# Kernel tuning notes

Hardware: AMD Instinct MI355X
Metric: run time of the kernel (lower is better)

The kernel has to match this reference:

```python
import jax, jax.numpy as jnp
import numpy as np
from jax import lax

EPS = 1e-5

def quantize_ternary(w):
    # scale = mean(|w|).clamp_min(1e-5) computed on detached weight
    scale = jnp.maximum(jnp.mean(jnp.abs(lax.stop_gradient(w))), EPS)
    ws = w / scale
    # STE: forward uses round+clamp, backward is identity in ws
    wq = lax.stop_gradient(jnp.clip(jnp.round(ws), -1.0, 1.0) - ws) + ws
    return wq * scale

def conv2d(x, w, b):
    # x: [N,C,H,W], w: [O,I,kh,kw], stride 1, pad 1 -> same spatial size
    out = lax.conv_general_dilated(
        x, w, window_strides=(1, 1), padding=[(1, 1), (1, 1)],
        dimension_numbers=("NCHW", "OIHW", "NCHW"))
    return out + b[None, :, None, None]

def setup_inputs() -> dict:
    key = jax.random.key(0)
    k1, k2, k3, k4, k5 = jax.random.split(key, 5)
    N, C_in, C_out, H, W, K = 16, 64, 64, 128, 128, 3
    fan_in = C_in * K * K
    bound = 1.0 / np.sqrt(fan_in)
    x = jax.random.normal(k1, (N, C_in, H, W), dtype=jnp.float32)
    w = jax.random.uniform(k2, (C_out, C_in, K, K), minval=-bound, maxval=bound, dtype=jnp.float32)
    b = jax.random.uniform(k3, (C_out,), minval=-bound, maxval=bound, dtype=jnp.float32)
    # growth child: kaiming-uniform-like init scaled by 0.01, zero bias
    w_child = jax.random.uniform(k4, (C_out, C_in, K, K), minval=-bound, maxval=bound, dtype=jnp.float32) * 0.01
    b_child = jnp.zeros((C_out,), dtype=jnp.float32)
    gate = jnp.zeros((1,), dtype=jnp.float32)  # growth_gate buffer
    return {"x": x, "w": w, "b": b, "w_child": w_child, "b_child": b_child, "gate": gate}

def reference(x, w, b, w_child, b_child, gate):
    out = conv2d(x, quantize_ternary(w), b)
    child_out = conv2d(x, quantize_ternary(w_child), b_child)
    g = jax.nn.sigmoid(gate)  # shape [1], broadcasts
    return out + g * child_out
```

## Files before the change

### kernel.cpp

```cpp
#include <hip/hip_runtime.h>
#include <math.h>


typedef __attribute__((ext_vector_type(8))) short short8;
typedef __attribute__((ext_vector_type(4))) float float4v;

__device__ inline unsigned short f2bf(float f) {
  union { float f; unsigned u; } v; v.f = f;
  unsigned u = v.u;
  return (unsigned short)((u + 0x7FFFu + ((u >> 16) & 1u)) >> 16);
}

__global__ __launch_bounds__(1024) void reduce_abs_part(const float* __restrict__ w,
                                                        const float* __restrict__ wc,
                                                        double* __restrict__ part) {
  const int base = blockIdx.x * 4096 + threadIdx.x;
  double a = 0.0, c = 0.0;
#pragma unroll
  for (int i = 0; i < 4; ++i) {
    a += (double)fabsf(w[base + i * 1024]);
    c += (double)fabsf(wc[base + i * 1024]);
  }
#pragma unroll
  for (int off = 32; off > 0; off >>= 1) {
    a += __shfl_down(a, off);
    c += __shfl_down(c, off);
  }
  __shared__ double sa[16], sc[16];
  int wv = threadIdx.x >> 6;
  if ((threadIdx.x & 63) == 0) { sa[wv] = a; sc[wv] = c; }
  __syncthreads();
  if (threadIdx.x == 0) {
    double ta = 0.0, tc = 0.0;
#pragma unroll
    for (int i = 0; i < 16; ++i) { ta += sa[i]; tc += sc[i]; }
    part[blockIdx.x] = ta;
    part[9 + blockIdx.x] = tc;
  }
}

__global__ void quant_combine(const float* __restrict__ w, const float* __restrict__ wc,
                              const float* __restrict__ b, const float* __restrict__ bc,
                              const float* __restrict__ gate, const double* __restrict__ part,
                              unsigned short* __restrict__ wq, float* __restrict__ beff) {
  double s0 = 0.0, s1 = 0.0;
#pragma unroll
  for (int i = 0; i < 9; ++i) { s0 += part[i]; s1 += part[9 + i]; }
  const float sw = fmaxf((float)(s0 * (1.0 / 36864.0)), 1e-5f);
  const float sc = fmaxf((float)(s1 * (1.0 / 36864.0)), 1e-5f);
  const float g = 1.0f / (1.0f + expf(-gate[0]));
  int idx = blockIdx.x * 256 + threadIdx.x;
  int tap = idx >> 12;
  int oc = (idx >> 6) & 63;
  int ci = idx & 63;
  int src = oc * 576 + ci * 9 + tap;
  float q1 = fminf(1.f, fmaxf(-1.f, rintf(w[src] / sw))) * sw;
  float q2 = fminf(1.f, fmaxf(-1.f, rintf(wc[src] / sc))) * sc;
  wq[idx] = f2bf(q1 + g * q2);
  if (idx < 64) beff[idx] = b[idx] + g * bc[idx];
}

__global__ __launch_bounds__(256, 2) void conv_fused(
    const float* __restrict__ x, const unsigned short* __restrict__ wq,
    const float* __restrict__ beff, float* __restrict__ out) {
  extern __shared__ __align__(16) char smem[];
  const int bid = blockIdx.x;
  const int xcd = bid & 7;
  const int u = bid >> 3;
  const int n = xcd * 2 + (u >> 6);
  const int h0 = (u & 63) * 2;
  const int tid = threadIdx.x;
  const int lane = tid & 63;
  const int wv = tid >> 6;
  const int rw = wv >> 1;
  const int pxh = (wv & 1) * 64;
  const int ln15 = lane & 15;
  const int lq = lane >> 4;
  const int koff = lq << 3;

  const float* xn = x + (size_t)n * (64 * 16384);

  if (tid < 64) {
    int r = tid >> 4;
    int q = (tid >> 1) & 7;
    int px = (tid & 1) * 129;
    int swz = q ^ (px & 7);
    *(short8*)(smem + ((r * 1040 + px * 8 + swz) << 4)) = (short8)0;
  }

  const int w128 = tid & 127;
  const int hi = tid >> 7;
#pragma unroll 4
  for (int pass = 0; pass < 16; ++pass) {
    const int c2 = pass * 2 + hi;
    const int r = c2 >> 3;
    const int q = c2 & 7;
    const int h = h0 + r - 1;
    short8 v = (short8)0;
    if ((unsigned)h < 128u) {
      const float* sp = xn + q * 8 * 16384 + h * 128 + w128;
      float f0 = sp[0 * 16384], f1 = sp[1 * 16384], f2 = sp[2 * 16384],
            f3 = sp[3 * 16384], f4 = sp[4 * 16384], f5 = sp[5 * 16384],
            f6 = sp[6 * 16384], f7 = sp[7 * 16384];
      v[0] = (short)f2bf(f0); v[1] = (short)f2bf(f1);
      v[2] = (short)f2bf(f2); v[3] = (short)f2bf(f3);
      v[4] = (short)f2bf(f4); v[5] = (short)f2bf(f5);
      v[6] = (short)f2bf(f6); v[7] = (short)f2bf(f7);
    }
    const int px = w128 + 1;
    const int swz = q ^ (px & 7);
    *(short8*)(smem + ((r * 1040 + px * 8 + swz) << 4)) = v;
  }
  __syncthreads();

  const unsigned short* wbase = wq + ln15 * 64 + koff;

  short8 A[2][2][4], B[2][2][4];
  float4v acc[4][4] = {};

  auto load_tap = [&](int tap, short8 Ab[2][4], short8 Bb[2][4]) {
    const int dh = tap / 3;
    const int dw = tap - dh * 3;
    const int r = rw + dh;
    const int pb = pxh + ln15 + dw;
    const int swz = lq ^ (pb & 7);
    const int b0 = ((r * 130 + pb) << 7) + (swz << 4);
    const unsigned short* wp = wbase + tap * 4096;
#pragma unroll
    for (int mf = 0; mf < 4; ++mf) {
      Ab[0][mf] = *(const short8*)(smem + (b0 + mf * 2048));
      Ab[1][mf] = *(const short8*)(smem + ((b0 ^ 64) + mf * 2048));
    }
#pragma unroll
    for (int qd = 0; qd < 4; ++qd) {
      Bb[0][qd] = *(const short8*)(wp + qd * 1024);
      Bb[1][qd] = *(const short8*)(wp + qd * 1024 + 32);
    }
  };

  load_tap(0, A[0], B[0]);
#pragma unroll
  for (int tap = 0; tap < 9; ++tap) {
    const int cur = tap & 1, nxt = cur ^ 1;
    if (tap < 8) load_tap(tap + 1, A[nxt], B[nxt]);
    __builtin_amdgcn_s_setprio(1);
#pragma unroll
    for (int cc2 = 0; cc2 < 2; ++cc2)
#pragma unroll
      for (int mf = 0; mf < 4; ++mf)
#pragma unroll
        for (int qd = 0; qd < 4; ++qd)
          acc[mf][qd] = __builtin_amdgcn_mfma_f32_16x16x32_bf16(
              A[cur][cc2][mf], B[cur][cc2][qd], acc[mf][qd], 0, 0, 0);
    __builtin_amdgcn_s_setprio(0);
  }

  const int rq = lane >> 4;
  float bias[4];
#pragma unroll
  for (int q = 0; q < 4; ++q) bias[q] = beff[q * 16 + ln15];
#pragma unroll
  for (int mf = 0; mf < 4; ++mf) {
#pragma unroll
    for (int qd = 0; qd < 4; ++qd) {
      float4v v = acc[mf][qd] + bias[qd];
      int oc = qd * 16 + ln15;
      float* op = out + (((n * 64 + oc) * 128 + h0 + rw) * 128 + pxh + mf * 16 + rq * 4);
      *(float4v*)op = v;
    }
  }
}

extern "C" void kernel_launch(void* const* d_in, const int* in_sizes, int n_in,
                              void* d_out, int out_size, void* d_ws, size_t ws_size,
                              hipStream_t stream) {
  const float* x = (const float*)d_in[0];
  const float* w = (const float*)d_in[1];
  const float* b = (const float*)d_in[2];
  const float* wc = (const float*)d_in[3];
  const float* bc = (const float*)d_in[4];
  const float* gate = (const float*)d_in[5];

  unsigned short* wq = (unsigned short*)d_ws;
  float* beff = (float*)((char*)d_ws + 73728);
  double* part = (double*)((char*)d_ws + 73984);

  reduce_abs_part<<<9, 1024, 0, stream>>>(w, wc, part);
  quant_combine<<<144, 256, 0, stream>>>(w, wc, b, bc, gate, part, wq, beff);
  conv_fused<<<16 * 64, 256, 66560, stream>>>(x, wq, beff, (float*)d_out);
}
```

Baseline: 165.8 us.

## Double block to 4 rows, stage weights through LDS with double buffering

Each block now covers 4 output rows with 512 threads (8 waves), which halves the grid and reduces halo re-reads of x. Per-tap weight fragments are loaded once per block into a swizzled, double-buffered LDS region and shared across waves, instead of each wave reading them directly from global memory. A __syncthreads per tap and roughly 115KB of LDS per block are added, which limits occupancy to about one block per CU, and the register-prefetched A fragments from the previous version are removed.

```diff
diff --git a/kernel.cpp b/kernel.cpp
--- a/kernel.cpp
+++ b/kernel.cpp
@@ -60,15 +60,18 @@
   if (idx < 64) beff[idx] = b[idx] + g * bc[idx];
 }
 
-__global__ __launch_bounds__(256, 2) void conv_fused(
+__global__ __launch_bounds__(512, 2) void conv_fused(
     const float* __restrict__ x, const unsigned short* __restrict__ wq,
     const float* __restrict__ beff, float* __restrict__ out) {
   extern __shared__ __align__(16) char smem[];
+  char* Abase = smem;
+  char* Bbase = smem + 99200;
+
   const int bid = blockIdx.x;
   const int xcd = bid & 7;
   const int u = bid >> 3;
-  const int n = xcd * 2 + (u >> 6);
-  const int h0 = (u & 63) * 2;
+  const int n = xcd * 2 + (u >> 5);
+  const int h0 = (u & 31) * 4;
   const int tid = threadIdx.x;
   const int lane = tid & 63;
   const int wv = tid >> 6;
@@ -76,73 +79,73 @@
   const int pxh = (wv & 1) * 64;
   const int ln15 = lane & 15;
   const int lq = lane >> 4;
-  const int koff = lq << 3;
 
   const float* xn = x + (size_t)n * (64 * 16384);
 
-  if (tid < 64) {
-    int r = tid >> 4;
-    int q = (tid >> 1) & 7;
-    int px = (tid & 1) * 129;
-    int swz = q ^ (px & 7);
-    *(short8*)(smem + ((r * 1040 + px * 8 + swz) << 4)) = (short8)0;
+  const short8 b0v = *(const short8*)(wq + tid * 8);
+
+  if (tid < 56) {
+    int slot = (tid < 48) ? ((tid >> 3) * 129 * 8 + (tid & 7)) : (6192 + (tid - 48));
+    *(short8*)(Abase + (slot << 4)) = (short8)0;
   }
 
   const int w128 = tid & 127;
   const int hi = tid >> 7;
 #pragma unroll 4
-  for (int pass = 0; pass < 16; ++pass) {
-    const int c2 = pass * 2 + hi;
-    const int r = c2 >> 3;
-    const int q = c2 & 7;
+  for (int pass = 0; pass < 12; ++pass) {
+    const int k = pass * 4 + hi;
+    const int r = k >> 3;
+    const int c = k & 7;
     const int h = h0 + r - 1;
     short8 v = (short8)0;
     if ((unsigned)h < 128u) {
-      const float* sp = xn + q * 8 * 16384 + h * 128 + w128;
-      float f0 = sp[0 * 16384], f1 = sp[1 * 16384], f2 = sp[2 * 16384],
-            f3 = sp[3 * 16384], f4 = sp[4 * 16384], f5 = sp[5 * 16384],
-            f6 = sp[6 * 16384], f7 = sp[7 * 16384];
-      v[0] = (short)f2bf(f0); v[1] = (short)f2bf(f1);
-      v[2] = (short)f2bf(f2); v[3] = (short)f2bf(f3);
-      v[4] = (short)f2bf(f4); v[5] = (short)f2bf(f5);
-      v[6] = (short)f2bf(f6); v[7] = (short)f2bf(f7);
+      const float* sp = xn + c * 8 * 16384 + h * 128 + w128;
+      v[0] = (short)f2bf(sp[0 * 16384]);
+      v[1] = (short)f2bf(sp[1 * 16384]);
+      v[2] = (short)f2bf(sp[2 * 16384]);
+      v[3] = (short)f2bf(sp[3 * 16384]);
+      v[4] = (short)f2bf(sp[4 * 16384]);
+      v[5] = (short)f2bf(sp[5 * 16384]);
+      v[6] = (short)f2bf(sp[6 * 16384]);
+      v[7] = (short)f2bf(sp[7 * 16384]);
     }
-    const int px = w128 + 1;
-    const int swz = q ^ (px & 7);
-    *(short8*)(smem + ((r * 1040 + px * 8 + swz) << 4)) = v;
+    const int p = w128 + 1;
+    const int slot = (r * 129 + p) * 8 + (c ^ (p & 7));
+    *(short8*)(Abase + (slot << 4)) = v;
   }
+
+  const int bslot = (tid & ~7) | ((tid & 7) ^ ((tid >> 3) & 7));
+  *(short8*)(Bbase + (bslot << 4)) = b0v;
   __syncthreads();
 
-  const unsigned short* wbase = wq + ln15 * 64 + koff;
-
-  short8 A[2][2][4], B[2][2][4];
   float4v acc[4][4] = {};
 
-  auto load_tap = [&](int tap, short8 Ab[2][4], short8 Bb[2][4]) {
+#pragma unroll
+  for (int tap = 0; tap < 9; ++tap) {
+    const int cb = tap & 1;
+    short8 btrans;
+    if (tap < 8) btrans = *(const short8*)(wq + (tap + 1) * 4096 + tid * 8);
+
     const int dh = tap / 3;
     const int dw = tap - dh * 3;
     const int r = rw + dh;
     const int pb = pxh + ln15 + dw;
-    const int swz = lq ^ (pb & 7);
-    const int b0 = ((r * 130 + pb) << 7) + (swz << 4);
-    const unsigned short* wp = wbase + tap * 4096;
+    const int a0 = (((r * 129 + pb) << 3) + (lq ^ (pb & 7))) << 4;
+    short8 Ab[2][4], Bb[2][4];
 #pragma unroll
     for (int mf = 0; mf < 4; ++mf) {
-      Ab[0][mf] = *(const short8*)(smem + (b0 + mf * 2048));
-      Ab[1][mf] = *(const short8*)(smem + ((b0 ^ 64) + mf * 2048));
+      Ab[0][mf] = *(const short8*)(Abase + (a0 + mf * 2048));
+      Ab[1][mf] = *(const short8*)(Abase + ((a0 ^ 64) + mf * 2048));
     }
 #pragma unroll
     for (int qd = 0; qd < 4; ++qd) {
-      Bb[0][qd] = *(const short8*)(wp + qd * 1024);
-      Bb[1][qd] = *(const short8*)(wp + qd * 1024 + 32);
+      const int oc = qd * 16 + ln15;
+      Bb[0][qd] = *(const short8*)(Bbase + cb * 8192 +
+                                   ((oc * 8 + (lq ^ (ln15 & 7))) << 4));
+      Bb[1][qd] = *(const short8*)(Bbase + cb * 8192 +
+                                   ((oc * 8 + ((lq + 4) ^ (ln15 & 7))) << 4));
     }
-  };
 
-  load_tap(0, A[0], B[0]);
-#pragma unroll
-  for (int tap = 0; tap < 9; ++tap) {
-    const int cur = tap & 1, nxt = cur ^ 1;
-    if (tap < 8) load_tap(tap + 1, A[nxt], B[nxt]);
     __builtin_amdgcn_s_setprio(1);
 #pragma unroll
     for (int cc2 = 0; cc2 < 2; ++cc2)
@@ -151,8 +154,13 @@
 #pragma unroll
         for (int qd = 0; qd < 4; ++qd)
           acc[mf][qd] = __builtin_amdgcn_mfma_f32_16x16x32_bf16(
-              A[cur][cc2][mf], B[cur][cc2][qd], acc[mf][qd], 0, 0, 0);
+              Ab[cc2][mf], Bb[cc2][qd], acc[mf][qd], 0, 0, 0);
     __builtin_amdgcn_s_setprio(0);
+
+    if (tap < 8) {
+      *(short8*)(Bbase + (cb ^ 1) * 8192 + (bslot << 4)) = btrans;
+      __syncthreads();
+    }
   }
 
   const int rq = lane >> 4;
@@ -187,5 +195,5 @@
 
   reduce_abs_part<<<9, 1024, 0, stream>>>(w, wc, part);
   quant_combine<<<144, 256, 0, stream>>>(w, wc, b, bc, gate, part, wq, beff);
-  conv_fused<<<16 * 64, 256, 66560, stream>>>(x, wq, beff, (float*)d_out);
+  conv_fused<<<512, 512, 115584, stream>>>(x, wq, beff, (float*)d_out);
 }
```

Result: faster. 144.0 us (-13.1%).
